# Performance work log

Hardware: AMD Instinct MI355X
Metric: run time of the kernel (lower is better)

Reference implementation:

```python
import jax, jax.numpy as jnp
import numpy as np

M, N, NUM_ITER, BATCH = 512, 2048, 16, 4096


def setup_inputs() -> dict:
    key = jax.random.key(0)
    k_y, k_D, k_thr = jax.random.split(key, 3)
    # Dictionary D (== A in the module), column-scaled like a sensing matrix
    D = np.asarray(jax.random.normal(k_D, (M, N), dtype=jnp.float32)) / np.sqrt(M)
    # W = inv(D D^T) D, then normalize columns so w_i . d_i == 1 (ALISTA analytic weight)
    W = np.linalg.inv(D @ D.T) @ D
    W = W / np.sum(W * D, axis=0, keepdims=True)
    y = jax.random.normal(k_y, (BATCH, M), dtype=jnp.float32)
    thr = jax.random.uniform(k_thr, (NUM_ITER,), dtype=jnp.float32) * 0.1  # positive thresholds
    step = jnp.ones((NUM_ITER,), dtype=jnp.float32)
    return {"y": y, "A": jnp.asarray(D), "W": jnp.asarray(W), "thr": thr, "step": step}


def reference(y, A, W, thr, step):
    # y: [B, m]; A, W: [m, n]; thr, step: [numIter]
    B = y.shape[0]
    n = A.shape[1]

    def body(d, ts):
        t, s = ts
        r = d @ A.T - y                      # [B, m]  == (A @ d.T - y.T).T
        z = d - s * (r @ W)                  # [B, n]  == (W.T @ r.T).T
        d_new = jnp.sign(z) * jnp.maximum(jnp.abs(z) - t, 0.0)  # soft threshold
        return d_new, d_new

    d0 = jnp.zeros((B, n), dtype=y.dtype)
    _, xs = jax.lax.scan(body, d0, (thr, step))
    return xs  # [numIter, B, n]: all intermediate iterates, like the returned list x
```

## Files before the change

### kernel.cpp

```cpp
#include <hip/hip_runtime.h>


#define NDIM 2048
#define MDIM 512
#define BATCHN 4096
#define NITER 16
#define BM 128
#define BN 128
#define BK 64

#define BM2 256
#define BN2 128
#define BK3 64
#define NK3 (NDIM / BK3)

typedef _Float16 f16;
typedef f16 f16x8 __attribute__((ext_vector_type(8)));
typedef float f32x4 __attribute__((ext_vector_type(4)));

__device__ __forceinline__ void gload_lds16(const void* g, void* lds) {
  __builtin_amdgcn_global_load_lds(
      (const __attribute__((address_space(1))) unsigned int*)g,
      (__attribute__((address_space(3))) unsigned int*)lds, 16, 0, 0);
}

__global__ __launch_bounds__(512, 2) void alista_iter_gemm(
    const f16* __restrict__ Ds, const f16* __restrict__ P,
    const f16* __restrict__ Ch,
    const float* __restrict__ thr, const float* __restrict__ step, int it,
    float sigma, float inv_sigma, float inv_sigma_next,
    float* __restrict__ outIter, f16* __restrict__ DsNext)
{
  __shared__ __align__(16) f16 ldsA[3 * BM2 * BK3];
  __shared__ __align__(16) f16 ldsB[3 * BN2 * BK3];

  const int tid = threadIdx.x;
  const int w = tid >> 6, l = tid & 63;
  const int wm = w >> 1, wn = w & 1;
  const int h = l >> 4;

  const int bid = blockIdx.x;
  const int wgid = (bid & 7) * 32 + (bid >> 3);
  const int rowTile = (wgid >> 4) * BM2;
  const int colTile = (wgid & 15) * BN2;

  const f16* Abase = Ds + (size_t)rowTile * NDIM;
  const f16* Bbase = P + (size_t)colTile * NDIM;

  auto stageA = [&](int buf, int t, int r) {
    int row = r * 64 + (tid >> 3);
    int gsw = ((tid & 7) ^ (row & 7)) << 4;
    gload_lds16((const char*)(Abase + (size_t)row * NDIM + t * BK3) + gsw,
                (char*)ldsA + buf * 32768 + r * 8192 + w * 1024);
  };
  auto stageB = [&](int buf, int t, int r) {
    int row = r * 64 + (tid >> 3);
    int gsw = ((tid & 7) ^ (row & 7)) << 4;
    gload_lds16((const char*)(Bbase + (size_t)row * NDIM + t * BK3) + gsw,
                (char*)ldsB + buf * 16384 + r * 8192 + w * 1024);
  };

#define READ8(bR, kh, af, bf)                                                   \
  {                                                                             \
    const f16* bA_ = ldsA + (bR) * 16384;                                       \
    const f16* bB_ = ldsB + (bR) * 8192;                                        \
    const int c_ = (kh) * 4 + h;                                                \
    _Pragma("unroll")                                                           \
    for (int m = 0; m < 4; ++m) {                                               \
      int row = wm * 64 + m * 16 + (l & 15);                                    \
      af[m] = *(const f16x8*)(bA_ + row * 64 + ((c_ ^ (row & 7)) << 3));        \
    }                                                                           \
    _Pragma("unroll")                                                           \
    for (int n = 0; n < 4; ++n) {                                               \
      int row = wn * 64 + n * 16 + (l & 15);                                    \
      bf[n] = *(const f16x8*)(bB_ + row * 64 + ((c_ ^ (row & 7)) << 3));        \
    }                                                                           \
  }

#define MFMA16(af, bf)                                                          \
  __builtin_amdgcn_s_setprio(1);                                                \
  _Pragma("unroll")                                                             \
  for (int m = 0; m < 4; ++m)                                                   \
    _Pragma("unroll")                                                           \
    for (int n = 0; n < 4; ++n)                                                 \
      acc[m][n] = __builtin_amdgcn_mfma_f32_16x16x32_f16(af[m], bf[n],          \
                                                         acc[m][n], 0, 0, 0);   \
  __builtin_amdgcn_s_setprio(0);

  f32x4 acc[4][4] = {};
  f16x8 af[4], bf[4];

#pragma unroll
  for (int r = 0; r < 4; ++r) stageA(0, 0, r);
#pragma unroll
  for (int r = 0; r < 2; ++r) stageB(0, 0, r);
#pragma unroll
  for (int r = 0; r < 4; ++r) stageA(1, 1, r);
#pragma unroll
  for (int r = 0; r < 2; ++r) stageB(1, 1, r);
  asm volatile("s_waitcnt vmcnt(6)" ::: "memory");
  __builtin_amdgcn_s_barrier();
  __builtin_amdgcn_sched_barrier(0);

  int bR = 0;
  int bS = 2;

  for (int t = 0; t < NK3; ++t) {
    const bool pf = (t + 2 < NK3);

    READ8(bR, 0, af, bf);
    if (pf) { stageA(bS, t + 2, 0); stageA(bS, t + 2, 1); stageB(bS, t + 2, 0); }
    __builtin_amdgcn_s_barrier();
    asm volatile("s_waitcnt lgkmcnt(0)" ::: "memory");
    __builtin_amdgcn_sched_barrier(0);
    MFMA16(af, bf);
    __builtin_amdgcn_s_barrier();

    READ8(bR, 1, af, bf);
    if (pf) { stageA(bS, t + 2, 2); stageA(bS, t + 2, 3); stageB(bS, t + 2, 1); }
    __builtin_amdgcn_s_barrier();
    asm volatile("s_waitcnt lgkmcnt(0)" ::: "memory");
    __builtin_amdgcn_sched_barrier(0);
    MFMA16(af, bf);
    if (pf) asm volatile("s_waitcnt vmcnt(6)" ::: "memory");
    else    asm volatile("s_waitcnt vmcnt(0)" ::: "memory");
    __builtin_amdgcn_s_barrier();
    __builtin_amdgcn_sched_barrier(0);

    bR = (bR == 2) ? 0 : bR + 1;
    bS = (bS == 2) ? 0 : bS + 1;
  }

  const int baseRow = rowTile + wm * 64 + (h << 2);
  const int baseCol = colTile + wn * 64 + (l & 15);
  const float s = step[it];
  const float tt = thr[it];
  const size_t itOff = (size_t)it * (size_t)BATCHN * NDIM;
#pragma unroll
  for (int m = 0; m < 4; ++m)
#pragma unroll
    for (int n = 0; n < 4; ++n)
#pragma unroll
      for (int r = 0; r < 4; ++r) {
        int row = baseRow + m * 16 + r;
        int col = baseCol + n * 16;
        size_t g = (size_t)row * NDIM + col;
        float v = acc[m][n][r];
        float ds = (float)Ds[g];
        float cv = (float)Ch[g];
        float z = sigma * (ds - s * (v - cv * inv_sigma));
        float az = __builtin_fabsf(z) - tt;
        float dn = az > 0.f ? (z > 0.f ? az : -az) : 0.f;
        outIter[itOff + g] = dn;
        DsNext[g] = (f16)(dn * inv_sigma_next);
      }
#undef READ8
#undef MFMA16
}

__global__ __launch_bounds__(256, 2) void gemm_pre(
    const f16* __restrict__ Ap, const f16* __restrict__ Bp, int K,
    f16* __restrict__ outH)
{
  __shared__ __align__(16) f16 ldsA[BM * BK];
  __shared__ __align__(16) f16 ldsB[BN * BK];
  int t = threadIdx.x;
  int w = t >> 6, l = t & 63;
  int wr = w >> 1, wc = w & 1;
  int rowTile = blockIdx.y * BM;
  int colTile = blockIdx.x * BN;

  f32x4 acc[4][4] = {};
  const f16* Arow = Ap + (size_t)rowTile * K;
  const f16* Brow = Bp + (size_t)colTile * K;
  for (int kt = 0; kt < K; kt += BK) {
    __syncthreads();
#pragma unroll
    for (int n = 0; n < 4; ++n) {
      int e = n * 2048 + t * 8;
      int r = e >> 6, c = e & 63;
      gload_lds16(Arow + (size_t)r * K + kt + c, (char*)ldsA + n * 4096 + w * 1024);
    }
#pragma unroll
    for (int n = 0; n < 4; ++n) {
      int e = n * 2048 + t * 8;
      int r = e >> 6, c = e & 63;
      gload_lds16(Brow + (size_t)r * K + kt + c, (char*)ldsB + n * 4096 + w * 1024);
    }
    asm volatile("s_waitcnt vmcnt(0)" ::: "memory");
    __syncthreads();
#pragma unroll
    for (int ks = 0; ks < 2; ++ks) {
      f16x8 a[4], b[4];
#pragma unroll
      for (int m = 0; m < 4; ++m)
        a[m] = *(const f16x8*)(ldsA + ((wr * 64 + m * 16 + (l & 15)) * BK + ks * 32 + (l >> 4) * 8));
#pragma unroll
      for (int n = 0; n < 4; ++n)
        b[n] = *(const f16x8*)(ldsB + ((wc * 64 + n * 16 + (l & 15)) * BK + ks * 32 + (l >> 4) * 8));
#pragma unroll
      for (int m = 0; m < 4; ++m)
#pragma unroll
        for (int n = 0; n < 4; ++n)
          acc[m][n] = __builtin_amdgcn_mfma_f32_16x16x32_f16(a[m], b[n], acc[m][n], 0, 0, 0);
    }
  }

  int baseRow = rowTile + wr * 64 + ((l >> 4) << 2);
  int baseCol = colTile + wc * 64 + (l & 15);
#pragma unroll
  for (int m = 0; m < 4; ++m)
#pragma unroll
    for (int n = 0; n < 4; ++n)
#pragma unroll
      for (int r = 0; r < 4; ++r) {
        size_t g = (size_t)(baseRow + m * 16 + r) * NDIM + baseCol + n * 16;
        outH[g] = (f16)acc[m][n][r];
      }
}

__global__ __launch_bounds__(256) void trans_h(
    const float* __restrict__ in, f16* __restrict__ oh)
{
  __shared__ float tile[64][65];
  int t = threadIdx.x;
  int tr = t >> 6;
  int tc = t & 63;
  int r0 = blockIdx.y * 64;
  int c0 = blockIdx.x * 64;
#pragma unroll
  for (int i = 0; i < 16; ++i) {
    int r = i * 4 + tr;
    tile[r][tc] = in[(size_t)(r0 + r) * NDIM + c0 + tc];
  }
  __syncthreads();
#pragma unroll
  for (int i = 0; i < 16; ++i) {
    int r = i * 4 + tr;
    oh[(size_t)(c0 + r) * MDIM + r0 + tc] = (f16)tile[tc][r];
  }
}

__global__ __launch_bounds__(256) void tofp16(
    const float* __restrict__ in, f16* __restrict__ oh)
{
  size_t i = (size_t)blockIdx.x * 256 + threadIdx.x;
  oh[i] = (f16)in[i];
}

__global__ __launch_bounds__(256) void alista_iter0(
    const f16* __restrict__ Ch, const float* __restrict__ thr,
    const float* __restrict__ step, float* __restrict__ out, f16* __restrict__ Ds1)
{
  size_t i = (size_t)blockIdx.x * 256 + threadIdx.x;
  float s = step[0], tt = thr[0];
  float z = s * (float)Ch[i];
  float az = __builtin_fabsf(z) - tt;
  float dn = az > 0.f ? (z > 0.f ? az : -az) : 0.f;
  out[i] = dn;
  Ds1[i] = (f16)dn;
}

extern "C" void kernel_launch(void* const* d_in, const int* in_sizes, int n_in,
                              void* d_out, int out_size, void* d_ws, size_t ws_size,
                              hipStream_t stream)
{
  const float* y    = (const float*)d_in[0];
  const float* A    = (const float*)d_in[1];
  const float* W    = (const float*)d_in[2];
  const float* thr  = (const float*)d_in[3];
  const float* step = (const float*)d_in[4];
  float* out = (float*)d_out;
  char* ws = (char*)d_ws;

  f16* Pht = (f16*)(ws + 0);
  f16* Ch  = (f16*)(ws + (8ull  << 20));
  f16* DsA = (f16*)(ws + (24ull << 20));
  f16* DsB = (f16*)(ws + (40ull << 20));
  f16* Wth = (f16*)(ws + (24ull << 20));
  f16* Ath = (f16*)(ws + (26ull << 20));
  f16* yh  = (f16*)(ws + (40ull << 20));

  trans_h<<<dim3(32, 8), 256, 0, stream>>>(A, Ath);
  trans_h<<<dim3(32, 8), 256, 0, stream>>>(W, Wth);
  tofp16<<<(BATCHN * MDIM) / 256, 256, 0, stream>>>(y, yh);

  gemm_pre<<<dim3(16, 16), 256, 0, stream>>>(Wth, Ath, MDIM, Pht);
  gemm_pre<<<dim3(16, 32), 256, 0, stream>>>(yh, Wth, MDIM, Ch);

  alista_iter0<<<(BATCHN * NDIM) / 256, 256, 0, stream>>>(Ch, thr, step, out, DsA);

  f16* cur = DsA;
  f16* nxt = DsB;
  float sigma = 1.0f;
  for (int it = 1; it < NITER; ++it) {
    alista_iter_gemm<<<dim3(256), 512, 0, stream>>>(
        cur, Pht, Ch, thr, step, it,
        sigma, 1.0f / sigma, 0.25f / sigma, out, nxt);
    sigma *= 4.0f;
    f16* tmp = cur; cur = nxt; nxt = tmp;
  }
}
```

Baseline: 750.8 us.

## Split K across wave pairs with LDS reduction to reuse B fragments

```diff
diff --git a/kernel.cpp b/kernel.cpp
--- a/kernel.cpp
+++ b/kernel.cpp
@@ -31,12 +31,15 @@
     float sigma, float inv_sigma, float inv_sigma_next,
     float* __restrict__ outIter, f16* __restrict__ DsNext)
 {
-  __shared__ __align__(16) f16 ldsA[3 * BM2 * BK3];
-  __shared__ __align__(16) f16 ldsB[3 * BN2 * BK3];
+  __shared__ __align__(16) f16 ldsAll[3 * BM2 * BK3 + 3 * BN2 * BK3];
+  f16* ldsA = ldsAll;
+  f16* ldsB = ldsAll + 3 * BM2 * BK3;
 
   const int tid = threadIdx.x;
   const int w = tid >> 6, l = tid & 63;
-  const int wm = w >> 1, wn = w & 1;
+  const int ks = w & 1;
+  const int wn = (w >> 1) & 1;
+  const int wm = w >> 2;
   const int h = l >> 4;
 
   const int bid = blockIdx.x;
@@ -60,16 +63,20 @@
                 (char*)ldsB + buf * 16384 + r * 8192 + w * 1024);
   };
 
-#define READ8(bR, kh, af, bf)                                                   \
+#define READ_A4(bR, mOfs, af)                                                   \
   {                                                                             \
     const f16* bA_ = ldsA + (bR) * 16384;                                       \
-    const f16* bB_ = ldsB + (bR) * 8192;                                        \
-    const int c_ = (kh) * 4 + h;                                                \
+    const int c_ = ks * 4 + h;                                                  \
     _Pragma("unroll")                                                           \
     for (int m = 0; m < 4; ++m) {                                               \
-      int row = wm * 64 + m * 16 + (l & 15);                                    \
+      int row = wm * 128 + ((mOfs) + m) * 16 + (l & 15);                        \
       af[m] = *(const f16x8*)(bA_ + row * 64 + ((c_ ^ (row & 7)) << 3));        \
     }                                                                           \
+  }
+#define READ_B4(bR, bf)                                                         \
+  {                                                                             \
+    const f16* bB_ = ldsB + (bR) * 8192;                                        \
+    const int c_ = ks * 4 + h;                                                  \
     _Pragma("unroll")                                                           \
     for (int n = 0; n < 4; ++n) {                                               \
       int row = wn * 64 + n * 16 + (l & 15);                                    \
@@ -77,17 +84,17 @@
     }                                                                           \
   }
 
-#define MFMA16(af, bf)                                                          \
+#define MFMA16(accOfs, af, bf)                                                  \
   __builtin_amdgcn_s_setprio(1);                                                \
   _Pragma("unroll")                                                             \
   for (int m = 0; m < 4; ++m)                                                   \
     _Pragma("unroll")                                                           \
     for (int n = 0; n < 4; ++n)                                                 \
-      acc[m][n] = __builtin_amdgcn_mfma_f32_16x16x32_f16(af[m], bf[n],          \
-                                                         acc[m][n], 0, 0, 0);   \
+      acc[(accOfs) + m][n] = __builtin_amdgcn_mfma_f32_16x16x32_f16(            \
+          af[m], bf[n], acc[(accOfs) + m][n], 0, 0, 0);                         \
   __builtin_amdgcn_s_setprio(0);
 
-  f32x4 acc[4][4] = {};
+  f32x4 acc[8][4] = {};
   f16x8 af[4], bf[4];
 
 #pragma unroll
@@ -108,20 +115,21 @@
   for (int t = 0; t < NK3; ++t) {
     const bool pf = (t + 2 < NK3);
 
-    READ8(bR, 0, af, bf);
+    READ_A4(bR, 0, af);
+    READ_B4(bR, bf);
     if (pf) { stageA(bS, t + 2, 0); stageA(bS, t + 2, 1); stageB(bS, t + 2, 0); }
     __builtin_amdgcn_s_barrier();
     asm volatile("s_waitcnt lgkmcnt(0)" ::: "memory");
     __builtin_amdgcn_sched_barrier(0);
-    MFMA16(af, bf);
+    MFMA16(0, af, bf);
     __builtin_amdgcn_s_barrier();
 
-    READ8(bR, 1, af, bf);
+    READ_A4(bR, 4, af);
     if (pf) { stageA(bS, t + 2, 2); stageA(bS, t + 2, 3); stageB(bS, t + 2, 1); }
     __builtin_amdgcn_s_barrier();
     asm volatile("s_waitcnt lgkmcnt(0)" ::: "memory");
     __builtin_amdgcn_sched_barrier(0);
-    MFMA16(af, bf);
+    MFMA16(4, af, bf);
     if (pf) asm volatile("s_waitcnt vmcnt(6)" ::: "memory");
     else    asm volatile("s_waitcnt vmcnt(0)" ::: "memory");
     __builtin_amdgcn_s_barrier();
@@ -131,30 +139,66 @@
     bS = (bS == 2) ? 0 : bS + 1;
   }
 
-  const int baseRow = rowTile + wm * 64 + (h << 2);
+  float* xb = (float*)ldsAll;
+  const int p = w >> 1;
+  const size_t sbase = (size_t)p * 8192 + (size_t)ks * 4096;
+  const size_t rbase = (size_t)p * 8192 + (size_t)(ks ^ 1) * 4096;
+  if (ks == 0) {
+#pragma unroll
+    for (int m4 = 0; m4 < 4; ++m4)
+#pragma unroll
+      for (int n = 0; n < 4; ++n)
+        *(f32x4*)(xb + sbase + l * 64 + (((m4 * 4 + n) ^ (l & 15)) << 2)) = acc[4 + m4][n];
+  } else {
+#pragma unroll
+    for (int m4 = 0; m4 < 4; ++m4)
+#pragma unroll
+      for (int n = 0; n < 4; ++n)
+        *(f32x4*)(xb + sbase + l * 64 + (((m4 * 4 + n) ^ (l & 15)) << 2)) = acc[m4][n];
+  }
+  __syncthreads();
+  if (ks == 0) {
+#pragma unroll
+    for (int m4 = 0; m4 < 4; ++m4)
+#pragma unroll
+      for (int n = 0; n < 4; ++n)
+        acc[m4][n] += *(const f32x4*)(xb + rbase + l * 64 + (((m4 * 4 + n) ^ (l & 15)) << 2));
+  } else {
+#pragma unroll
+    for (int m4 = 0; m4 < 4; ++m4)
+#pragma unroll
+      for (int n = 0; n < 4; ++n)
+        acc[4 + m4][n] += *(const f32x4*)(xb + rbase + l * 64 + (((m4 * 4 + n) ^ (l & 15)) << 2));
+  }
+
+  const int baseRow = rowTile + wm * 128 + ks * 64 + (h << 2);
   const int baseCol = colTile + wn * 64 + (l & 15);
   const float s = step[it];
   const float tt = thr[it];
   const size_t itOff = (size_t)it * (size_t)BATCHN * NDIM;
-#pragma unroll
-  for (int m = 0; m < 4; ++m)
-#pragma unroll
-    for (int n = 0; n < 4; ++n)
-#pragma unroll
-      for (int r = 0; r < 4; ++r) {
-        int row = baseRow + m * 16 + r;
-        int col = baseCol + n * 16;
-        size_t g = (size_t)row * NDIM + col;
-        float v = acc[m][n][r];
-        float ds = (float)Ds[g];
-        float cv = (float)Ch[g];
-        float z = sigma * (ds - s * (v - cv * inv_sigma));
-        float az = __builtin_fabsf(z) - tt;
-        float dn = az > 0.f ? (z > 0.f ? az : -az) : 0.f;
-        outIter[itOff + g] = dn;
-        DsNext[g] = (f16)(dn * inv_sigma_next);
+#define EPILOG(ACCOFS)                                                          \
+  _Pragma("unroll")                                                             \
+  for (int m4 = 0; m4 < 4; ++m4)                                                \
+    _Pragma("unroll")                                                           \
+    for (int n = 0; n < 4; ++n)                                                 \
+      _Pragma("unroll")                                                         \
+      for (int r = 0; r < 4; ++r) {                                             \
+        int row = baseRow + m4 * 16 + r;                                        \
+        int col = baseCol + n * 16;                                             \
+        size_t g = (size_t)row * NDIM + col;                                    \
+        float v = acc[(ACCOFS) + m4][n][r];                                     \
+        float ds = (float)Ds[g];                                                \
+        float cv = (float)Ch[g];                                                \
+        float z = sigma * (ds - s * (v - cv * inv_sigma));                      \
+        float az = __builtin_fabsf(z) - tt;                                     \
+        float dn = az > 0.f ? (z > 0.f ? az : -az) : 0.f;                       \
+        outIter[itOff + g] = dn;                                                \
+        DsNext[g] = (f16)(dn * inv_sigma_next);                                 \
       }
-#undef READ8
+  if (ks == 0) { EPILOG(0) } else { EPILOG(4) }
+#undef EPILOG
+#undef READ_A4
+#undef READ_B4
 #undef MFMA16
 }
 
```

After: 745.9 us. No clear change (-0.6%).
